# Kernel optimization log

Hardware: AMD Instinct MI355X
Metric: run time of the kernel (lower is better)

The kernel has to match this reference:

```python
import jax, jax.numpy as jnp
import numpy as np

N = 50000    # nodes
E = 800000   # edges (avg degree 16)
IN = 256     # in_dim
HID = 256    # hidden_dim
OUT = 128    # out_dim


def setup_inputs() -> dict:
    key = jax.random.key(0)
    ks = jax.random.split(key, 9)
    features = jax.random.normal(ks[0], (N, IN), jnp.float32)
    src = jax.random.randint(ks[1], (E,), 0, N, jnp.int32)
    dst = jax.random.randint(ks[2], (E,), 0, N, jnp.int32)
    noise = jax.random.normal(ks[3], (N, OUT), jnp.float32)
    def glorot(k, shape, fan):
        return jax.random.normal(k, shape, jnp.float32) / np.float32(np.sqrt(fan))
    W1 = glorot(ks[4], (IN, HID), IN);  b1 = jnp.zeros((HID,), jnp.float32)
    W2 = glorot(ks[5], (HID, OUT), HID); b2 = jnp.zeros((OUT,), jnp.float32)
    W3 = glorot(ks[6], (HID, OUT), HID); b3 = jnp.zeros((OUT,), jnp.float32)
    fcW = glorot(ks[7], (HID, IN), IN)   # nn.Linear(in_dim, hidden_dim).weight: [HID, IN]
    return dict(features=features, noise=noise, W1=W1, b1=b1, W2=W2, b2=b2,
                W3=W3, b3=b3, fcW=fcW, src=src, dst=dst)


def _gcn(x, W, b, src, dst, out_norm, in_norm):
    """DGL GraphConv norm='both': D_out^{-1/2} A D_in^{-1/2} X W + b."""
    x = x * out_norm[:, None]          # scale src features by out-deg^{-1/2}
    x = x @ W                          # dense transform (order commutes with SpMM)
    agg = jax.ops.segment_sum(x[src], dst, num_segments=N)  # sparse aggregate
    return agg * in_norm[:, None] + b


def reference(features, noise, W1, b1, W2, b2, W3, b3, fcW, src, dst):
    ones = jnp.ones((E,), jnp.float32)
    out_deg = jax.ops.segment_sum(ones, src, num_segments=N)
    in_deg = jax.ops.segment_sum(ones, dst, num_segments=N)
    out_norm = jnp.maximum(out_deg, 1.0) ** -0.5
    in_norm = jnp.maximum(in_deg, 1.0) ** -0.5

    h = jax.nn.relu(_gcn(features, W1, b1, src, dst, out_norm, in_norm))
    mean = jax.nn.relu(_gcn(h, W2, b2, src, dst, out_norm, in_norm))
    log_std = _gcn(h, W3, b3, src, dst, out_norm, in_norm)  # identity activation
    z = mean + noise * jnp.exp(log_std)
    seq_fts = features @ fcW.T
    return z, h, seq_fts
```

## Files before the change

kernel.cpp:

```cpp
#include <hip/hip_runtime.h>
#include <hip/hip_bf16.h>
#include <stdint.h>
#include <math.h>

#define IN_DIM 256
#define HID_DIM 256
#define OUT_DIM 128

typedef __attribute__((ext_vector_type(8))) short short8;
typedef __attribute__((ext_vector_type(4))) float floatx4;

__device__ __forceinline__ float bf2f(ushort u) {
  union { uint32_t i; float f; } v; v.i = ((uint32_t)u) << 16; return v.f;
}
__device__ __forceinline__ ushort f2bf(float f) {
  union { float f; uint32_t u; } v; v.f = f;
  uint32_t u = v.u;
  uint32_t r = u + 0x7fffu + ((u >> 16) & 1u);
  return (ushort)(r >> 16);
}

__global__ void deg_kernel(const int* __restrict__ src, const int* __restrict__ dst,
                           int* __restrict__ out_deg, int* __restrict__ in_deg, int E) {
  int e = (blockIdx.x * 256 + threadIdx.x) * 2;
  if (e + 1 < E) {
    int2 s = *(const int2*)(src + e);
    int2 d = *(const int2*)(dst + e);
    atomicAdd(&out_deg[s.x], 1);
    atomicAdd(&out_deg[s.y], 1);
    atomicAdd(&in_deg[d.x], 1);
    atomicAdd(&in_deg[d.y], 1);
  } else if (e < E) {
    atomicAdd(&out_deg[src[e]], 1);
    atomicAdd(&in_deg[dst[e]], 1);
  }
}

__global__ __launch_bounds__(1024) void scan_kernel(const int* __restrict__ deg,
                                                    int* __restrict__ row_ptr, int n) {
  __shared__ int lds[1024];
  int t = threadIdx.x;
  const int CH = 64;
  int base = t * CH;
  int v[CH];
  int s = 0;
#pragma unroll
  for (int j = 0; j < CH / 4; ++j) {
    int idx = base + j * 4;
    int4 q = make_int4(0, 0, 0, 0);
    if (idx + 3 < n) {
      q = *(const int4*)(deg + idx);
    } else {
      if (idx < n)     q.x = deg[idx];
      if (idx + 1 < n) q.y = deg[idx + 1];
      if (idx + 2 < n) q.z = deg[idx + 2];
    }
    v[j * 4 + 0] = q.x; v[j * 4 + 1] = q.y; v[j * 4 + 2] = q.z; v[j * 4 + 3] = q.w;
    s += q.x + q.y + q.z + q.w;
  }
  lds[t] = s;
  __syncthreads();
  for (int off = 1; off < 1024; off <<= 1) {
    int add = (t >= off) ? lds[t - off] : 0;
    __syncthreads();
    lds[t] += add;
    __syncthreads();
  }
  int run = lds[t] - s;
  if (t == 0) row_ptr[0] = 0;
#pragma unroll
  for (int j = 0; j < CH; ++j) {
    int idx = base + j;
    run += v[j];
    if (idx < n) row_ptr[idx + 1] = run;
  }
}

__global__ void fill_kernel(const int* __restrict__ src, const int* __restrict__ dst,
                            const int* __restrict__ row_ptr, int* __restrict__ fill_cnt,
                            const int* __restrict__ out_deg,
                            int2* __restrict__ edge_sw, int E) {
  int e = (blockIdx.x * 256 + threadIdx.x) * 2;
  if (e + 1 < E) {
    int2 s = *(const int2*)(src + e);
    int2 d = *(const int2*)(dst + e);
    int pos0 = row_ptr[d.x] + atomicAdd(&fill_cnt[d.x], 1);
    int od0 = out_deg[s.x]; if (od0 < 1) od0 = 1;
    int2 r0; r0.x = s.x; r0.y = __float_as_int(rsqrtf((float)od0));
    edge_sw[pos0] = r0;
    int pos1 = row_ptr[d.y] + atomicAdd(&fill_cnt[d.y], 1);
    int od1 = out_deg[s.y]; if (od1 < 1) od1 = 1;
    int2 r1; r1.x = s.y; r1.y = __float_as_int(rsqrtf((float)od1));
    edge_sw[pos1] = r1;
  } else if (e < E) {
    int d = dst[e]; int s = src[e];
    int pos = row_ptr[d] + atomicAdd(&fill_cnt[d], 1);
    int od = out_deg[s]; if (od < 1) od = 1;
    int2 r; r.x = s; r.y = __float_as_int(rsqrtf((float)od));
    edge_sw[pos] = r;
  }
}

__global__ void prep_weights(const float* __restrict__ W1, const float* __restrict__ W2,
                             const float* __restrict__ W3, const float* __restrict__ b2,
                             const float* __restrict__ b3, const float* __restrict__ fcW,
                             ushort* __restrict__ W1T, ushort* __restrict__ WcT,
                             float* __restrict__ bcat, ushort* __restrict__ fcWb) {
  int k = blockIdx.x;
  int n = threadIdx.x;
  W1T[n * 256 + k] = f2bf(W1[k * 256 + n]);
  WcT[n * 256 + k] = f2bf((n < 128) ? W2[k * 128 + n] : W3[k * 128 + (n - 128)]);
  fcWb[k * 256 + n] = f2bf(fcW[k * 256 + n]);
  if (k == 0) bcat[n] = (n < 128) ? b2[n] : b3[n - 128];
}

__global__ __launch_bounds__(256) void agg_kernel(
    const ushort* __restrict__ x, const int* __restrict__ row_ptr,
    const int2* __restrict__ edge_sw, ushort* __restrict__ out, int N) {
  int wave = threadIdx.x >> 6, lane = threadIdx.x & 63;
  int n = blockIdx.x * 4 + wave;
  if (n >= N) return;
  int half = lane >> 5;
  int hl = lane & 31;
  int start = row_ptr[n], end = row_ptr[n + 1];
  int dg = end - start; if (dg < 1) dg = 1;
  float inn = rsqrtf((float)dg);

  float acc[8];
#pragma unroll
  for (int k = 0; k < 8; ++k) acc[k] = 0.f;

  for (int base = start; base < end; base += 16) {
    int cs[8]; float cw[8];
#pragma unroll
    for (int k = 0; k < 8; ++k) {
      int i = base + half + 2 * k;
      cs[k] = 0; cw[k] = 0.f;
      if (i < end) { int2 e = edge_sw[i]; cs[k] = e.x; cw[k] = __int_as_float(e.y); }
    }
    uint4 v[8];
#pragma unroll
    for (int k = 0; k < 8; ++k)
      v[k] = *(const uint4*)&x[(size_t)cs[k] * 256 + hl * 8];
#pragma unroll
    for (int k = 0; k < 8; ++k) {
      const uint32_t* p = (const uint32_t*)&v[k];
      float wk = cw[k];
#pragma unroll
      for (int q = 0; q < 4; ++q) {
        acc[2 * q]     += bf2f((ushort)(p[q] & 0xffffu)) * wk;
        acc[2 * q + 1] += bf2f((ushort)(p[q] >> 16)) * wk;
      }
    }
  }

#pragma unroll
  for (int k = 0; k < 8; ++k) acc[k] += __shfl_xor(acc[k], 32, 64);

  if (half == 0) {
    uint4 o;
    uint32_t* po = (uint32_t*)&o;
#pragma unroll
    for (int q = 0; q < 4; ++q) {
      po[q] = ((uint32_t)f2bf(acc[2 * q + 1] * inn) << 16) |
              (uint32_t)f2bf(acc[2 * q] * inn);
    }
    *(uint4*)&out[(size_t)n * 256 + hl * 8] = o;
  }
}

__global__ __launch_bounds__(256, 2) void gemm_kernel(
    const ushort* __restrict__ A, const float* __restrict__ A32,
    const ushort* __restrict__ BT,
    const float* __restrict__ bias, const float* __restrict__ noise,
    float* __restrict__ C32, ushort* __restrict__ Cbf, int M, int mode) {
  __shared__ alignas(16) ushort A_lds[128 * 72];
  __shared__ alignas(16) ushort B_lds[256 * 72];
  int t = threadIdx.x;
  int m0 = blockIdx.x * 128;
  int wave = t >> 6, lane = t & 63;
  int wm = wave * 32;
  int l15 = lane & 15, quad = lane >> 4;

  floatx4 acc[2][16];
#pragma unroll
  for (int i = 0; i < 2; ++i)
#pragma unroll
    for (int j = 0; j < 16; ++j) acc[i][j] = (floatx4)(0.f);

  for (int kc = 0; kc < 256; kc += 64) {
    if (mode == 2) {
#pragma unroll
      for (int r = 0; r < 8; ++r) {
        int idx = t + r * 256;
        int row = idx >> 4;
        int c = (idx & 15) << 2;
        int grow = m0 + row; if (grow > M - 1) grow = M - 1;
        float4 v = *(const float4*)(A32 + (size_t)grow * 256 + kc + c);
        ushort4 o;
        o.x = f2bf(v.x); o.y = f2bf(v.y); o.z = f2bf(v.z); o.w = f2bf(v.w);
        *(ushort4*)&A_lds[row * 72 + c] = o;
        *(ushort4*)(Cbf + (size_t)grow * 256 + kc + c) = o;
      }
    } else {
#pragma unroll
      for (int r = 0; r < 4; ++r) {
        int idx = t + r * 256;
        int row = idx >> 3;
        int c = (idx & 7) << 3;
        int grow = m0 + row; if (grow > M - 1) grow = M - 1;
        *(uint4*)&A_lds[row * 72 + c] = *(const uint4*)(A + (size_t)grow * 256 + kc + c);
      }
    }
#pragma unroll
    for (int r = 0; r < 8; ++r) {
      int idx = t + r * 256;
      int row = idx >> 3;
      int c = (idx & 7) << 3;
      *(uint4*)&B_lds[row * 72 + c] = *(const uint4*)(BT + (size_t)row * 256 + kc + c);
    }
    __syncthreads();
#pragma unroll
    for (int ko = 0; ko < 2; ++ko) {
      short8 a[2];
#pragma unroll
      for (int i = 0; i < 2; ++i)
        a[i] = *(const short8*)&A_lds[(wm + i * 16 + l15) * 72 + ko * 32 + quad * 8];
#pragma unroll
      for (int j = 0; j < 16; ++j) {
        short8 b = *(const short8*)&B_lds[(j * 16 + l15) * 72 + ko * 32 + quad * 8];
#pragma unroll
        for (int i = 0; i < 2; ++i)
          acc[i][j] = __builtin_amdgcn_mfma_f32_16x16x32_bf16(a[i], b, acc[i][j], 0, 0, 0);
      }
    }
    __syncthreads();
  }

  if (mode == 1) {
#pragma unroll
    for (int i = 0; i < 2; ++i) {
#pragma unroll
      for (int j = 0; j < 8; ++j) {
        int col = j * 16 + l15;
        float bm = bias[col];
        float bl = bias[col + 128];
#pragma unroll
        for (int r = 0; r < 4; ++r) {
          int row = m0 + wm + i * 16 + quad * 4 + r;
          if (row < M) {
            float mean = acc[i][j][r] + bm;
            float ls = acc[i][j + 8][r] + bl;
            size_t o = (size_t)row * 128 + col;
            C32[o] = fmaxf(mean, 0.f) + noise[o] * expf(ls);
          }
        }
      }
    }
  } else {
#pragma unroll
    for (int i = 0; i < 2; ++i) {
#pragma unroll
      for (int j = 0; j < 16; ++j) {
        int col = j * 16 + l15;
        float bv = (mode == 0) ? bias[col] : 0.f;
#pragma unroll
        for (int r = 0; r < 4; ++r) {
          int row = m0 + wm + i * 16 + quad * 4 + r;
          if (row < M) {
            float v = acc[i][j][r] + bv;
            if (mode == 0) v = fmaxf(v, 0.f);
            size_t o = (size_t)row * 256 + col;
            C32[o] = v;
            if (mode == 0) Cbf[o] = f2bf(v);
          }
        }
      }
    }
  }
}

extern "C" void kernel_launch(void* const* d_in, const int* in_sizes, int n_in,
                              void* d_out, int out_size, void* d_ws, size_t ws_size,
                              hipStream_t stream) {
  const float* features = (const float*)d_in[0];
  const float* noise    = (const float*)d_in[1];
  const float* W1 = (const float*)d_in[2];
  const float* b1 = (const float*)d_in[3];
  const float* W2 = (const float*)d_in[4];
  const float* b2 = (const float*)d_in[5];
  const float* W3 = (const float*)d_in[6];
  const float* b3 = (const float*)d_in[7];
  const float* fcW = (const float*)d_in[8];
  const int* src = (const int*)d_in[9];
  const int* dst = (const int*)d_in[10];
  const int N = in_sizes[0] / IN_DIM;
  const int E = in_sizes[9];

  float* out = (float*)d_out;
  float* z_out = out;
  float* h_out = out + (size_t)N * OUT_DIM;
  float* s_out = h_out + (size_t)N * HID_DIM;

  char* w = (char*)d_ws;
  auto carve = [&](size_t bytes) {
    char* p = w;
    w += (bytes + 255) & ~(size_t)255;
    return p;
  };
  ushort* feat_bf = (ushort*)carve((size_t)N * 256 * 2);
  ushort* h_bf    = (ushort*)carve((size_t)N * 256 * 2);
  ushort* agg_buf = (ushort*)carve((size_t)N * 256 * 2);
  ushort* W1T  = (ushort*)carve(256 * 256 * 2);
  ushort* WcT  = (ushort*)carve(256 * 256 * 2);
  ushort* fcWb = (ushort*)carve(256 * 256 * 2);
  float*  bcat = (float*)carve(256 * 4);
  int* degs    = (int*)carve((size_t)3 * N * 4);
  int* out_deg = degs;
  int* in_deg  = degs + N;
  int* fill_cnt = degs + 2 * N;
  int* row_ptr  = (int*)carve((size_t)(N + 1) * 4);
  int2* edge_sw = (int2*)carve((size_t)E * 8);

  hipMemsetAsync(degs, 0, (size_t)3 * N * 4, stream);
  int eblocks = ((E + 1) / 2 + 255) / 256;
  deg_kernel<<<eblocks, 256, 0, stream>>>(src, dst, out_deg, in_deg, E);
  scan_kernel<<<1, 1024, 0, stream>>>(in_deg, row_ptr, N);
  fill_kernel<<<eblocks, 256, 0, stream>>>(src, dst, row_ptr, fill_cnt, out_deg,
                                           edge_sw, E);

  prep_weights<<<256, 256, 0, stream>>>(W1, W2, W3, b2, b3, fcW, W1T, WcT, bcat, fcWb);

  int gblocks = (N + 127) / 128;
  gemm_kernel<<<gblocks, 256, 0, stream>>>((const ushort*)nullptr, features, fcWb,
                                           (const float*)nullptr, (const float*)nullptr,
                                           s_out, feat_bf, N, 2);
  agg_kernel<<<(N + 3) / 4, 256, 0, stream>>>(feat_bf, row_ptr, edge_sw, agg_buf, N);
  gemm_kernel<<<gblocks, 256, 0, stream>>>(agg_buf, (const float*)nullptr, W1T, b1,
                                           (const float*)nullptr, h_out, h_bf, N, 0);
  agg_kernel<<<(N + 3) / 4, 256, 0, stream>>>(h_bf, row_ptr, edge_sw, agg_buf, N);
  gemm_kernel<<<gblocks, 256, 0, stream>>>(agg_buf, (const float*)nullptr, WcT, bcat,
                                           noise, z_out, (ushort*)nullptr, N, 1);
}
```

Measured before the change: 587.7 us.

## Fuse neighbor aggregation into GEMM via LDS-resident aggregated tile

Replaces the separate aggregation kernel plus GEMM with a fused kernel. Each block aggregates 128 nodes' neighbor features into a swizzled 64KB LDS tile, then multiplies by the weight matrix read directly from global memory. This removes the intermediate aggregation buffer write and read and two launches. The cost is far fewer blocks and each wave serially processing 32 nodes, which reduces gather parallelism and latency hiding. B fragments are no longer staged in LDS.

Result: slower. 683.2 us (+16.2%).

```diff
diff --git a/kernel.cpp b/kernel.cpp
--- a/kernel.cpp
+++ b/kernel.cpp
@@ -114,66 +114,139 @@
   if (k == 0) bcat[n] = (n < 128) ? b2[n] : b3[n - 128];
 }
 
-__global__ __launch_bounds__(256) void agg_kernel(
+__global__ __launch_bounds__(256, 2) void gcn_fused_kernel(
     const ushort* __restrict__ x, const int* __restrict__ row_ptr,
-    const int2* __restrict__ edge_sw, ushort* __restrict__ out, int N) {
-  int wave = threadIdx.x >> 6, lane = threadIdx.x & 63;
-  int n = blockIdx.x * 4 + wave;
-  if (n >= N) return;
-  int half = lane >> 5;
-  int hl = lane & 31;
-  int start = row_ptr[n], end = row_ptr[n + 1];
-  int dg = end - start; if (dg < 1) dg = 1;
-  float inn = rsqrtf((float)dg);
-
-  float acc[8];
-#pragma unroll
-  for (int k = 0; k < 8; ++k) acc[k] = 0.f;
-
-  for (int base = start; base < end; base += 16) {
-    int cs[8]; float cw[8];
-#pragma unroll
-    for (int k = 0; k < 8; ++k) {
-      int i = base + half + 2 * k;
-      cs[k] = 0; cw[k] = 0.f;
-      if (i < end) { int2 e = edge_sw[i]; cs[k] = e.x; cw[k] = __int_as_float(e.y); }
-    }
-    uint4 v[8];
-#pragma unroll
-    for (int k = 0; k < 8; ++k)
-      v[k] = *(const uint4*)&x[(size_t)cs[k] * 256 + hl * 8];
-#pragma unroll
-    for (int k = 0; k < 8; ++k) {
-      const uint32_t* p = (const uint32_t*)&v[k];
-      float wk = cw[k];
-#pragma unroll
-      for (int q = 0; q < 4; ++q) {
-        acc[2 * q]     += bf2f((ushort)(p[q] & 0xffffu)) * wk;
-        acc[2 * q + 1] += bf2f((ushort)(p[q] >> 16)) * wk;
-      }
-    }
-  }
-
-#pragma unroll
-  for (int k = 0; k < 8; ++k) acc[k] += __shfl_xor(acc[k], 32, 64);
-
-  if (half == 0) {
-    uint4 o;
-    uint32_t* po = (uint32_t*)&o;
-#pragma unroll
-    for (int q = 0; q < 4; ++q) {
-      po[q] = ((uint32_t)f2bf(acc[2 * q + 1] * inn) << 16) |
-              (uint32_t)f2bf(acc[2 * q] * inn);
-    }
-    *(uint4*)&out[(size_t)n * 256 + hl * 8] = o;
+    const int2* __restrict__ edge_sw, const ushort* __restrict__ BT,
+    const float* __restrict__ bias, const float* __restrict__ noise,
+    float* __restrict__ C32, ushort* __restrict__ Cbf, int N, int mode) {
+  __shared__ alignas(16) ushort A_lds[128 * 256];
+  int t = threadIdx.x;
+  int wave = t >> 6, lane = t & 63;
+  int wm = wave * 32;
+  int m0 = blockIdx.x * 128;
+  int half = lane >> 5, hl = lane & 31;
+
+  int rp = 0;
+  if (lane < 33) {
+    int idx = m0 + wm + lane;
+    rp = row_ptr[idx < N ? idx : N];
+  }
+
+  for (int r = 0; r < 32; ++r) {
+    int start = __shfl(rp, r, 64);
+    int end   = __shfl(rp, r + 1, 64);
+    float ag[8];
+#pragma unroll
+    for (int k = 0; k < 8; ++k) ag[k] = 0.f;
+    int dg = end - start;
+    float inn = rsqrtf((float)(dg < 1 ? 1 : dg));
+
+    for (int base = start; base < end; base += 16) {
+      int cs[8]; float cw[8];
+#pragma unroll
+      for (int k = 0; k < 8; ++k) {
+        int i = base + half + 2 * k;
+        cs[k] = 0; cw[k] = 0.f;
+        if (i < end) { int2 e = edge_sw[i]; cs[k] = e.x; cw[k] = __int_as_float(e.y); }
+      }
+      uint4 v[8];
+#pragma unroll
+      for (int k = 0; k < 8; ++k)
+        v[k] = *(const uint4*)&x[(size_t)cs[k] * 256 + hl * 8];
+#pragma unroll
+      for (int k = 0; k < 8; ++k) {
+        const uint32_t* p = (const uint32_t*)&v[k];
+        float wk = cw[k];
+#pragma unroll
+        for (int q = 0; q < 4; ++q) {
+          ag[2 * q]     += bf2f((ushort)(p[q] & 0xffffu)) * wk;
+          ag[2 * q + 1] += bf2f((ushort)(p[q] >> 16)) * wk;
+        }
+      }
+    }
+#pragma unroll
+    for (int k = 0; k < 8; ++k) ag[k] += __shfl_xor(ag[k], 32, 64);
+
+    if (half == 0) {
+      uint4 o; uint32_t* po = (uint32_t*)&o;
+#pragma unroll
+      for (int q = 0; q < 4; ++q)
+        po[q] = ((uint32_t)f2bf(ag[2 * q + 1] * inn) << 16) |
+                (uint32_t)f2bf(ag[2 * q] * inn);
+      int col = (hl * 8) ^ ((r & 7) << 3);
+      *(uint4*)&A_lds[(wm + r) * 256 + col] = o;
+    }
+  }
+
+  int l15 = lane & 15, quad = lane >> 4;
+  floatx4 acc[2][16];
+#pragma unroll
+  for (int i = 0; i < 2; ++i)
+#pragma unroll
+    for (int j = 0; j < 16; ++j) acc[i][j] = (floatx4)(0.f);
+
+  for (int kq = 0; kq < 8; ++kq) {
+    short8 a[2];
+#pragma unroll
+    for (int i = 0; i < 2; ++i) {
+      int row = wm + i * 16 + l15;
+      int col = (kq * 32 + quad * 8) ^ ((l15 & 7) << 3);
+      a[i] = *(const short8*)&A_lds[row * 256 + col];
+    }
+#pragma unroll
+    for (int j = 0; j < 16; ++j) {
+      short8 b = *(const short8*)&BT[(size_t)(j * 16 + l15) * 256 + kq * 32 + quad * 8];
+#pragma unroll
+      for (int i = 0; i < 2; ++i)
+        acc[i][j] = __builtin_amdgcn_mfma_f32_16x16x32_bf16(a[i], b, acc[i][j], 0, 0, 0);
+    }
+  }
+
+  if (mode == 1) {
+#pragma unroll
+    for (int i = 0; i < 2; ++i) {
+#pragma unroll
+      for (int j = 0; j < 8; ++j) {
+        int col = j * 16 + l15;
+        float bm = bias[col];
+        float bl = bias[col + 128];
+#pragma unroll
+        for (int r = 0; r < 4; ++r) {
+          int row = m0 + wm + i * 16 + quad * 4 + r;
+          if (row < N) {
+            float mean = acc[i][j][r] + bm;
+            float ls = acc[i][j + 8][r] + bl;
+            size_t o = (size_t)row * 128 + col;
+            C32[o] = fmaxf(mean, 0.f) + noise[o] * expf(ls);
+          }
+        }
+      }
+    }
+  } else {
+#pragma unroll
+    for (int i = 0; i < 2; ++i) {
+#pragma unroll
+      for (int j = 0; j < 16; ++j) {
+        int col = j * 16 + l15;
+        float bv = bias[col];
+#pragma unroll
+        for (int r = 0; r < 4; ++r) {
+          int row = m0 + wm + i * 16 + quad * 4 + r;
+          if (row < N) {
+            float v = fmaxf(acc[i][j][r] + bv, 0.f);
+            size_t o = (size_t)row * 256 + col;
+            C32[o] = v;
+            Cbf[o] = f2bf(v);
+          }
+        }
+      }
+    }
   }
 }
 
 __global__ __launch_bounds__(256, 2) void gemm_kernel(
-    const ushort* __restrict__ A, const float* __restrict__ A32,
-    const ushort* __restrict__ BT,
-    const float* __restrict__ bias, const float* __restrict__ noise,
-    float* __restrict__ C32, ushort* __restrict__ Cbf, int M, int mode) {
+    const float* __restrict__ A32, const ushort* __restrict__ BT,
+    float* __restrict__ C32, ushort* __restrict__ Cbf, int M) {
   __shared__ alignas(16) ushort A_lds[128 * 72];
   __shared__ alignas(16) ushort B_lds[256 * 72];
   int t = threadIdx.x;
@@ -189,28 +262,17 @@
     for (int j = 0; j < 16; ++j) acc[i][j] = (floatx4)(0.f);
 
   for (int kc = 0; kc < 256; kc += 64) {
-    if (mode == 2) {
-#pragma unroll
-      for (int r = 0; r < 8; ++r) {
-        int idx = t + r * 256;
-        int row = idx >> 4;
-        int c = (idx & 15) << 2;
-        int grow = m0 + row; if (grow > M - 1) grow = M - 1;
-        float4 v = *(const float4*)(A32 + (size_t)grow * 256 + kc + c);
-        ushort4 o;
-        o.x = f2bf(v.x); o.y = f2bf(v.y); o.z = f2bf(v.z); o.w = f2bf(v.w);
-        *(ushort4*)&A_lds[row * 72 + c] = o;
-        *(ushort4*)(Cbf + (size_t)grow * 256 + kc + c) = o;
-      }
-    } else {
-#pragma unroll
-      for (int r = 0; r < 4; ++r) {
-        int idx = t + r * 256;
-        int row = idx >> 3;
-        int c = (idx & 7) << 3;
-        int grow = m0 + row; if (grow > M - 1) grow = M - 1;
-        *(uint4*)&A_lds[row * 72 + c] = *(const uint4*)(A + (size_t)grow * 256 + kc + c);
-      }
+#pragma unroll
+    for (int r = 0; r < 8; ++r) {
+      int idx = t + r * 256;
+      int row = idx >> 4;
+      int c = (idx & 15) << 2;
+      int grow = m0 + row; if (grow > M - 1) grow = M - 1;
+      float4 v = *(const float4*)(A32 + (size_t)grow * 256 + kc + c);
+      ushort4 o;
+      o.x = f2bf(v.x); o.y = f2bf(v.y); o.z = f2bf(v.z); o.w = f2bf(v.w);
+      *(ushort4*)&A_lds[row * 72 + c] = o;
+      *(ushort4*)(Cbf + (size_t)grow * 256 + kc + c) = o;
     }
 #pragma unroll
     for (int r = 0; r < 8; ++r) {
@@ -237,43 +299,17 @@
     __syncthreads();
   }
 
-  if (mode == 1) {
-#pragma unroll
-    for (int i = 0; i < 2; ++i) {
-#pragma unroll
-      for (int j = 0; j < 8; ++j) {
-        int col = j * 16 + l15;
-        float bm = bias[col];
-        float bl = bias[col + 128];
-#pragma unroll
-        for (int r = 0; r < 4; ++r) {
-          int row = m0 + wm + i * 16 + quad * 4 + r;
-          if (row < M) {
-            float mean = acc[i][j][r] + bm;
-            float ls = acc[i][j + 8][r] + bl;
-            size_t o = (size_t)row * 128 + col;
-            C32[o] = fmaxf(mean, 0.f) + noise[o] * expf(ls);
-          }
-        }
-      }
-    }
-  } else {
-#pragma unroll
-    for (int i = 0; i < 2; ++i) {
-#pragma unroll
-      for (int j = 0; j < 16; ++j) {
-        int col = j * 16 + l15;
-        float bv = (mode == 0) ? bias[col] : 0.f;
-#pragma unroll
-        for (int r = 0; r < 4; ++r) {
-          int row = m0 + wm + i * 16 + quad * 4 + r;
-          if (row < M) {
-            float v = acc[i][j][r] + bv;
-            if (mode == 0) v = fmaxf(v, 0.f);
-            size_t o = (size_t)row * 256 + col;
-            C32[o] = v;
-            if (mode == 0) Cbf[o] = f2bf(v);
-          }
+#pragma unroll
+  for (int i = 0; i < 2; ++i) {
+#pragma unroll
+    for (int j = 0; j < 16; ++j) {
+      int col = j * 16 + l15;
+#pragma unroll
+      for (int r = 0; r < 4; ++r) {
+        int row = m0 + wm + i * 16 + quad * 4 + r;
+        if (row < M) {
+          size_t o = (size_t)row * 256 + col;
+          C32[o] = acc[i][j][r];
         }
       }
     }
@@ -310,7 +346,6 @@
   };
   ushort* feat_bf = (ushort*)carve((size_t)N * 256 * 2);
   ushort* h_bf    = (ushort*)carve((size_t)N * 256 * 2);
-  ushort* agg_buf = (ushort*)carve((size_t)N * 256 * 2);
   ushort* W1T  = (ushort*)carve(256 * 256 * 2);
   ushort* WcT  = (ushort*)carve(256 * 256 * 2);
   ushort* fcWb = (ushort*)carve(256 * 256 * 2);
@@ -332,13 +367,9 @@
   prep_weights<<<256, 256, 0, stream>>>(W1, W2, W3, b2, b3, fcW, W1T, WcT, bcat, fcWb);
 
   int gblocks = (N + 127) / 128;
-  gemm_kernel<<<gblocks, 256, 0, stream>>>((const ushort*)nullptr, features, fcWb,
-                                           (const float*)nullptr, (const float*)nullptr,
-                                           s_out, feat_bf, N, 2);
-  agg_kernel<<<(N + 3) / 4, 256, 0, stream>>>(feat_bf, row_ptr, edge_sw, agg_buf, N);
-  gemm_kernel<<<gblocks, 256, 0, stream>>>(agg_buf, (const float*)nullptr, W1T, b1,
-                                           (const float*)nullptr, h_out, h_bf, N, 0);
-  agg_kernel<<<(N + 3) / 4, 256, 0, stream>>>(h_bf, row_ptr, edge_sw, agg_buf, N);
-  gemm_kernel<<<gblocks, 256, 0, stream>>>(agg_buf, (const float*)nullptr, WcT, bcat,
-                                           noise, z_out, (ushort*)nullptr, N, 1);
-}
+  gemm_kernel<<<gblocks, 256, 0, stream>>>(features, fcWb, s_out, feat_bf, N);
+  gcn_fused_kernel<<<gblocks, 256, 0, stream>>>(feat_bf, row_ptr, edge_sw, W1T, b1,
+                                                (const float*)nullptr, h_out, h_bf, N, 0);
+  gcn_fused_kernel<<<gblocks, 256, 0, stream>>>(h_bf, row_ptr, edge_sw, WcT, bcat,
+                                                noise, z_out, (ushort*)nullptr, N, 1);
+}
```

## Merge scan, weight prep and feature GEMM into one heterogeneous launch

Applied to the files above, without the earlier changes.

Folds the single-block degree scan, the weight transpose/convert kernel and the seq_fts GEMM into one kernel whose blocks are dispatched by blockIdx role. The feature GEMM now converts fcW to bf16 directly while loading it into LDS, and the 1024-thread serial scan becomes a 256-thread block running concurrently with the GEMM blocks. The goal is to remove launches and let the serial scan hide behind GEMM work. It also adds a fast path in the aggregation edge loads for full 16-edge chunks. The cost is redundant fcW conversion in every GEMM block, and a scan block with longer per-thread serial loops that may become the tail.

New measurement: 593.5 us. No clear change (+1.0%).

```diff
diff --git a/kernel.cpp b/kernel.cpp
--- a/kernel.cpp
+++ b/kernel.cpp
@@ -36,43 +36,115 @@
   }
 }
 
-__global__ __launch_bounds__(1024) void scan_kernel(const int* __restrict__ deg,
-                                                    int* __restrict__ row_ptr, int n) {
-  __shared__ int lds[1024];
+__global__ __launch_bounds__(256, 2) void mega_kernel(
+    const float* __restrict__ A32, const float* __restrict__ fcW,
+    float* __restrict__ C32, ushort* __restrict__ Cbf, int M,
+    const float* __restrict__ W1, const float* __restrict__ W2,
+    const float* __restrict__ W3, const float* __restrict__ b2,
+    const float* __restrict__ b3,
+    ushort* __restrict__ W1T, ushort* __restrict__ WcT, float* __restrict__ bcat,
+    const int* __restrict__ in_deg, int* __restrict__ row_ptr, int n,
+    int gblocks) {
+  __shared__ alignas(16) ushort A_lds[128 * 72];
+  __shared__ alignas(16) ushort B_lds[256 * 72];
+  int b = blockIdx.x;
   int t = threadIdx.x;
-  const int CH = 64;
-  int base = t * CH;
-  int v[CH];
-  int s = 0;
-#pragma unroll
-  for (int j = 0; j < CH / 4; ++j) {
-    int idx = base + j * 4;
-    int4 q = make_int4(0, 0, 0, 0);
-    if (idx + 3 < n) {
-      q = *(const int4*)(deg + idx);
-    } else {
-      if (idx < n)     q.x = deg[idx];
-      if (idx + 1 < n) q.y = deg[idx + 1];
-      if (idx + 2 < n) q.z = deg[idx + 2];
-    }
-    v[j * 4 + 0] = q.x; v[j * 4 + 1] = q.y; v[j * 4 + 2] = q.z; v[j * 4 + 3] = q.w;
-    s += q.x + q.y + q.z + q.w;
-  }
-  lds[t] = s;
-  __syncthreads();
-  for (int off = 1; off < 1024; off <<= 1) {
-    int add = (t >= off) ? lds[t - off] : 0;
+
+  if (b < gblocks) {
+    int m0 = b * 128;
+    int wave = t >> 6, lane = t & 63;
+    int wm = wave * 32;
+    int l15 = lane & 15, quad = lane >> 4;
+
+    floatx4 acc[2][16];
+#pragma unroll
+    for (int i = 0; i < 2; ++i)
+#pragma unroll
+      for (int j = 0; j < 16; ++j) acc[i][j] = (floatx4)(0.f);
+
+    for (int kc = 0; kc < 256; kc += 64) {
+#pragma unroll
+      for (int r = 0; r < 8; ++r) {
+        int idx = t + r * 256;
+        int row = idx >> 4;
+        int c = (idx & 15) << 2;
+        int grow = m0 + row; if (grow > M - 1) grow = M - 1;
+        float4 v = *(const float4*)(A32 + (size_t)grow * 256 + kc + c);
+        ushort4 o;
+        o.x = f2bf(v.x); o.y = f2bf(v.y); o.z = f2bf(v.z); o.w = f2bf(v.w);
+        *(ushort4*)&A_lds[row * 72 + c] = o;
+        *(ushort4*)(Cbf + (size_t)grow * 256 + kc + c) = o;
+      }
+#pragma unroll
+      for (int r = 0; r < 16; ++r) {
+        int idx = t + r * 256;
+        int row = idx >> 4;
+        int c = (idx & 15) << 2;
+        float4 v = *(const float4*)(fcW + (size_t)row * 256 + kc + c);
+        ushort4 o;
+        o.x = f2bf(v.x); o.y = f2bf(v.y); o.z = f2bf(v.z); o.w = f2bf(v.w);
+        *(ushort4*)&B_lds[row * 72 + c] = o;
+      }
+      __syncthreads();
+#pragma unroll
+      for (int ko = 0; ko < 2; ++ko) {
+        short8 a[2];
+#pragma unroll
+        for (int i = 0; i < 2; ++i)
+          a[i] = *(const short8*)&A_lds[(wm + i * 16 + l15) * 72 + ko * 32 + quad * 8];
+#pragma unroll
+        for (int j = 0; j < 16; ++j) {
+          short8 bb = *(const short8*)&B_lds[(j * 16 + l15) * 72 + ko * 32 + quad * 8];
+#pragma unroll
+          for (int i = 0; i < 2; ++i)
+            acc[i][j] = __builtin_amdgcn_mfma_f32_16x16x32_bf16(a[i], bb, acc[i][j], 0, 0, 0);
+        }
+      }
+      __syncthreads();
+    }
+
+#pragma unroll
+    for (int i = 0; i < 2; ++i) {
+#pragma unroll
+      for (int j = 0; j < 16; ++j) {
+        int col = j * 16 + l15;
+#pragma unroll
+        for (int r = 0; r < 4; ++r) {
+          int row = m0 + wm + i * 16 + quad * 4 + r;
+          if (row < M) {
+            size_t o = (size_t)row * 256 + col;
+            C32[o] = acc[i][j][r];
+          }
+        }
+      }
+    }
+  } else if (b < gblocks + 256) {
+    int k = b - gblocks;
+    int nn = t;
+    W1T[nn * 256 + k] = f2bf(W1[k * 256 + nn]);
+    WcT[nn * 256 + k] = f2bf((nn < 128) ? W2[k * 128 + nn] : W3[k * 128 + (nn - 128)]);
+    if (k == 0) bcat[nn] = (nn < 128) ? b2[nn] : b3[nn - 128];
+  } else {
+    int* lds = (int*)A_lds;
+    const int CH = (n + 255) / 256;
+    int base = t * CH;
+    int lim = base + CH; if (lim > n) lim = n;
+    int s = 0;
+    for (int i = base; i < lim; ++i) s += in_deg[i];
+    lds[t] = s;
     __syncthreads();
-    lds[t] += add;
-    __syncthreads();
-  }
-  int run = lds[t] - s;
-  if (t == 0) row_ptr[0] = 0;
-#pragma unroll
-  for (int j = 0; j < CH; ++j) {
-    int idx = base + j;
-    run += v[j];
-    if (idx < n) row_ptr[idx + 1] = run;
+    for (int off = 1; off < 256; off <<= 1) {
+      int add = (t >= off) ? lds[t - off] : 0;
+      __syncthreads();
+      lds[t] += add;
+      __syncthreads();
+    }
+    int run = lds[t] - s;
+    if (t == 0) row_ptr[0] = 0;
+    for (int i = base; i < lim; ++i) {
+      run += in_deg[i];
+      row_ptr[i + 1] = run;
+    }
   }
 }
 
@@ -101,19 +173,6 @@
   }
 }
 
-__global__ void prep_weights(const float* __restrict__ W1, const float* __restrict__ W2,
-                             const float* __restrict__ W3, const float* __restrict__ b2,
-                             const float* __restrict__ b3, const float* __restrict__ fcW,
-                             ushort* __restrict__ W1T, ushort* __restrict__ WcT,
-                             float* __restrict__ bcat, ushort* __restrict__ fcWb) {
-  int k = blockIdx.x;
-  int n = threadIdx.x;
-  W1T[n * 256 + k] = f2bf(W1[k * 256 + n]);
-  WcT[n * 256 + k] = f2bf((n < 128) ? W2[k * 128 + n] : W3[k * 128 + (n - 128)]);
-  fcWb[k * 256 + n] = f2bf(fcW[k * 256 + n]);
-  if (k == 0) bcat[n] = (n < 128) ? b2[n] : b3[n - 128];
-}
-
 __global__ __launch_bounds__(256) void agg_kernel(
     const ushort* __restrict__ x, const int* __restrict__ row_ptr,
     const int2* __restrict__ edge_sw, ushort* __restrict__ out, int N) {
@@ -132,11 +191,19 @@
 
   for (int base = start; base < end; base += 16) {
     int cs[8]; float cw[8];
-#pragma unroll
-    for (int k = 0; k < 8; ++k) {
-      int i = base + half + 2 * k;
-      cs[k] = 0; cw[k] = 0.f;
-      if (i < end) { int2 e = edge_sw[i]; cs[k] = e.x; cw[k] = __int_as_float(e.y); }
+    if (base + 16 <= end) {
+#pragma unroll
+      for (int k = 0; k < 8; ++k) {
+        int2 e = edge_sw[base + half + 2 * k];
+        cs[k] = e.x; cw[k] = __int_as_float(e.y);
+      }
+    } else {
+#pragma unroll
+      for (int k = 0; k < 8; ++k) {
+        int i = base + half + 2 * k;
+        cs[k] = 0; cw[k] = 0.f;
+        if (i < end) { int2 e = edge_sw[i]; cs[k] = e.x; cw[k] = __int_as_float(e.y); }
+      }
     }
     uint4 v[8];
 #pragma unroll
@@ -170,8 +237,7 @@
 }
 
 __global__ __launch_bounds__(256, 2) void gemm_kernel(
-    const ushort* __restrict__ A, const float* __restrict__ A32,
-    const ushort* __restrict__ BT,
+    const ushort* __restrict__ A, const ushort* __restrict__ BT,
     const float* __restrict__ bias, const float* __restrict__ noise,
     float* __restrict__ C32, ushort* __restrict__ Cbf, int M, int mode) {
   __shared__ alignas(16) ushort A_lds[128 * 72];
@@ -189,28 +255,13 @@
     for (int j = 0; j < 16; ++j) acc[i][j] = (floatx4)(0.f);
 
   for (int kc = 0; kc < 256; kc += 64) {
-    if (mode == 2) {
-#pragma unroll
-      for (int r = 0; r < 8; ++r) {
-        int idx = t + r * 256;
-        int row = idx >> 4;
-        int c = (idx & 15) << 2;
-        int grow = m0 + row; if (grow > M - 1) grow = M - 1;
-        float4 v = *(const float4*)(A32 + (size_t)grow * 256 + kc + c);
-        ushort4 o;
-        o.x = f2bf(v.x); o.y = f2bf(v.y); o.z = f2bf(v.z); o.w = f2bf(v.w);
-        *(ushort4*)&A_lds[row * 72 + c] = o;
-        *(ushort4*)(Cbf + (size_t)grow * 256 + kc + c) = o;
-      }
-    } else {
-#pragma unroll
-      for (int r = 0; r < 4; ++r) {
-        int idx = t + r * 256;
-        int row = idx >> 3;
-        int c = (idx & 7) << 3;
-        int grow = m0 + row; if (grow > M - 1) grow = M - 1;
-        *(uint4*)&A_lds[row * 72 + c] = *(const uint4*)(A + (size_t)grow * 256 + kc + c);
-      }
+#pragma unroll
+    for (int r = 0; r < 4; ++r) {
+      int idx = t + r * 256;
+      int row = idx >> 3;
+      int c = (idx & 7) << 3;
+      int grow = m0 + row; if (grow > M - 1) grow = M - 1;
+      *(uint4*)&A_lds[row * 72 + c] = *(const uint4*)(A + (size_t)grow * 256 + kc + c);
     }
 #pragma unroll
     for (int r = 0; r < 8; ++r) {
@@ -263,16 +314,15 @@
 #pragma unroll
       for (int j = 0; j < 16; ++j) {
         int col = j * 16 + l15;
-        float bv = (mode == 0) ? bias[col] : 0.f;
+        float bv = bias[col];
 #pragma unroll
         for (int r = 0; r < 4; ++r) {
           int row = m0 + wm + i * 16 + quad * 4 + r;
           if (row < M) {
-            float v = acc[i][j][r] + bv;
-            if (mode == 0) v = fmaxf(v, 0.f);
+            float v = fmaxf(acc[i][j][r] + bv, 0.f);
             size_t o = (size_t)row * 256 + col;
             C32[o] = v;
-            if (mode == 0) Cbf[o] = f2bf(v);
+            Cbf[o] = f2bf(v);
           }
         }
       }
@@ -313,7 +363,6 @@
   ushort* agg_buf = (ushort*)carve((size_t)N * 256 * 2);
   ushort* W1T  = (ushort*)carve(256 * 256 * 2);
   ushort* WcT  = (ushort*)carve(256 * 256 * 2);
-  ushort* fcWb = (ushort*)carve(256 * 256 * 2);
   float*  bcat = (float*)carve(256 * 4);
   int* degs    = (int*)carve((size_t)3 * N * 4);
   int* out_deg = degs;
@@ -325,20 +374,20 @@
   hipMemsetAsync(degs, 0, (size_t)3 * N * 4, stream);
   int eblocks = ((E + 1) / 2 + 255) / 256;
   deg_kernel<<<eblocks, 256, 0, stream>>>(src, dst, out_deg, in_deg, E);
-  scan_kernel<<<1, 1024, 0, stream>>>(in_deg, row_ptr, N);
+
+  int gblocks = (N + 127) / 128;
+  mega_kernel<<<gblocks + 257, 256, 0, stream>>>(
+      features, fcW, s_out, feat_bf, N,
+      W1, W2, W3, b2, b3, W1T, WcT, bcat,
+      in_deg, row_ptr, N, gblocks);
+
   fill_kernel<<<eblocks, 256, 0, stream>>>(src, dst, row_ptr, fill_cnt, out_deg,
                                            edge_sw, E);
 
-  prep_weights<<<256, 256, 0, stream>>>(W1, W2, W3, b2, b3, fcW, W1T, WcT, bcat, fcWb);
-
-  int gblocks = (N + 127) / 128;
-  gemm_kernel<<<gblocks, 256, 0, stream>>>((const ushort*)nullptr, features, fcWb,
-                                           (const float*)nullptr, (const float*)nullptr,
-                                           s_out, feat_bf, N, 2);
   agg_kernel<<<(N + 3) / 4, 256, 0, stream>>>(feat_bf, row_ptr, edge_sw, agg_buf, N);
-  gemm_kernel<<<gblocks, 256, 0, stream>>>(agg_buf, (const float*)nullptr, W1T, b1,
-                                           (const float*)nullptr, h_out, h_bf, N, 0);
+  gemm_kernel<<<gblocks, 256, 0, stream>>>(agg_buf, W1T, b1, (const float*)nullptr,
+                                           h_out, h_bf, N, 0);
   agg_kernel<<<(N + 3) / 4, 256, 0, stream>>>(h_bf, row_ptr, edge_sw, agg_buf, N);
-  gemm_kernel<<<gblocks, 256, 0, stream>>>(agg_buf, (const float*)nullptr, WcT, bcat,
-                                           noise, z_out, (ushort*)nullptr, N, 1);
-}
+  gemm_kernel<<<gblocks, 256, 0, stream>>>(agg_buf, WcT, bcat, noise,
+                                           z_out, (ushort*)nullptr, N, 1);
+}
```
